# Performance work log

Hardware: AMD Instinct MI355X
Metric: run time of the kernel (lower is better)

The kernel has to match this reference:

```python
import jax, jax.numpy as jnp
import numpy as np

EPS = 1e-5
NEG_SLOPE = 0.01


def _bn(h, gamma, beta):
    # Training-mode batch norm over axis 0 (biased variance, like torch)
    m = h.mean(axis=0)
    v = h.var(axis=0)
    return (h - m) * jax.lax.rsqrt(v + EPS) * gamma + beta


def setup_inputs() -> dict:
    N, F, H, C = 2048, 64, 128, 2
    key = jax.random.key(0)
    ks = jax.random.split(key, 12)
    g = lambda k, shp: jax.random.normal(k, shp, dtype=jnp.float32) * 0.05
    return {
        "x": jax.random.normal(ks[0], (N, F), dtype=jnp.float32),
        "node_features": jax.random.uniform(ks[1], (N, F), dtype=jnp.float32),
        "W1": g(ks[2], (F, H)), "b1": jnp.zeros((H,), jnp.float32),
        "g1": jnp.ones((H,), jnp.float32), "be1": jnp.zeros((H,), jnp.float32),
        "W2": g(ks[3], (H, H)), "b2": jnp.zeros((H,), jnp.float32),
        "g2": jnp.ones((H,), jnp.float32), "be2": jnp.zeros((H,), jnp.float32),
        "W3": g(ks[4], (H, F)), "b3": jnp.zeros((F,), jnp.float32),
        "W5": g(ks[5], (F, H)), "b5": jnp.zeros((H,), jnp.float32),
        "g5": jnp.ones((H,), jnp.float32), "be5": jnp.zeros((H,), jnp.float32),
        "W6": g(ks[6], (H, C)), "b6": jnp.zeros((C,), jnp.float32),
    }


def reference(x, node_features, W1, b1, g1, be1, W2, b2, g2, be2, W3, b3,
              W5, b5, g5, be5, W6, b6):
    N = node_features.shape[0]
    C = W6.shape[1]
    # static upper-triangular edge list == torch.combinations(arange(N), r=2)
    ei, ej = np.triu_indices(N, k=1)

    h = node_features
    xinit = h
    h = _bn(jax.nn.leaky_relu(h @ W1 + b1, NEG_SLOPE), g1, be1)
    h = _bn(jax.nn.leaky_relu(h @ W2 + b2, NEG_SLOPE), g2, be2)
    h = h @ W3 + b3 + xinit  # [N, F]

    # edge prediction: gather pairs, elementwise mult, MLP+BN+softmax
    e = h[ei] * h[ej]  # [E, F]
    e = _bn(jax.nn.leaky_relu(e @ W5 + b5, NEG_SLOPE), g5, be5)
    edge_pred = jax.nn.softmax(e @ W6 + b6, axis=-1)  # [E, C]

    probs = jnp.zeros((N, N, C), dtype=edge_pred.dtype)
    probs = probs.at[ei, ej].set(edge_pred).at[ej, ei].set(edge_pred)
    return probs
```

## Files before the change

### kernel.cpp

```cpp
#include <hip/hip_runtime.h>
#include <hip/hip_bf16.h>


typedef short short8 __attribute__((ext_vector_type(8)));
typedef float floatx4 __attribute__((ext_vector_type(4)));
typedef float float2v __attribute__((ext_vector_type(2)));

#define NN 2048
#define EPSV 1e-5f
#define EDGEF 2096128.f

__device__ __forceinline__ float bf2f(short s) {
    return __uint_as_float(((unsigned)(unsigned short)s) << 16);
}
__device__ __forceinline__ short f2bf(float f) {
    unsigned u = __float_as_uint(f);
    unsigned r = (u + 0x7FFFu + ((u >> 16) & 1u)) >> 16;
    return (short)r;
}
__device__ __forceinline__ float lrelu(float x) { return fmaxf(x, 0.01f * x); }
__device__ __forceinline__ float2v lrelu2(float2v z) {
    float2v r; r.x = fmaxf(z.x, 0.01f * z.x); r.y = fmaxf(z.y, 0.01f * z.y);
    return r;
}
__device__ __forceinline__ float2v fma2(float2v a, float2v b, float2v c) {
    float2v r; r.x = fmaf(a.x, b.x, c.x); r.y = fmaf(a.y, b.y, c.y); return r;
}

__device__ __forceinline__ int physB(int h, int f) {
    return ((((h >> 4) * 2 + (f >> 5)) * 64 + ((f >> 3) & 3) * 16 + (h & 15)) * 8) + (f & 7);
}

__device__ __forceinline__ void decode_tile(int bid, int& i0, int& j0, bool& str) {
    int s = bid >> 3, m = 0;
#pragma unroll 1
    while (s >= 32 - m) { s -= 32 - m; ++m; }
    i0 = ((bid & 7) + (m << 3)) * 8;
    j0 = (m + s) * 64;
    str = (s == 0);
}

__global__ __launch_bounds__(256) void k_l1(const float* __restrict__ nf,
                                            const float* __restrict__ W1,
                                            const float* __restrict__ b1,
                                            const float* __restrict__ W5,
                                            float* __restrict__ act1,
                                            float* __restrict__ stat1,
                                            short* __restrict__ w5bf) {
    __shared__ float xl[8 * 64];
    __shared__ float sS[128], sQ[128];
    int t = threadIdx.x, n0 = blockIdx.x * 8;
    if (blockIdx.x < 32) {
        int idx = blockIdx.x * 256 + t;
        w5bf[physB(idx & 127, idx >> 7)] = f2bf(W5[idx]);
    }
    if (t < 128) { sS[t] = 0.f; sQ[t] = 0.f; }
    xl[t] = nf[(size_t)n0 * 64 + t];
    xl[t + 256] = nf[(size_t)n0 * 64 + t + 256];
    __syncthreads();
    int nl = t >> 5, h0 = (t & 31) * 4;
    float acc[4];
    for (int k = 0; k < 4; ++k) acc[k] = b1[h0 + k];
    for (int f = 0; f < 64; ++f) {
        float r = xl[nl * 64 + f];
        const float* wr = W1 + f * 128 + h0;
        for (int k = 0; k < 4; ++k) acc[k] = fmaf(r, wr[k], acc[k]);
    }
    for (int k = 0; k < 4; ++k) {
        float a = lrelu(acc[k]);
        act1[(size_t)(n0 + nl) * 128 + h0 + k] = a;
        atomicAdd(&sS[h0 + k], a);
        atomicAdd(&sQ[h0 + k], a * a);
    }
    __syncthreads();
    if (t < 128) atomicAdd(&stat1[t], sS[t]);
    else atomicAdd(&stat1[t], sQ[t - 128]);
}

__global__ __launch_bounds__(256) void k_l2(const float* __restrict__ act1,
                                            const float* __restrict__ stat1,
                                            const float* __restrict__ g1,
                                            const float* __restrict__ be1,
                                            const float* __restrict__ W2,
                                            const float* __restrict__ b2,
                                            float* __restrict__ act2,
                                            float* __restrict__ stat2) {
    __shared__ float a1n[8 * 128];
    __shared__ float sS[128], sQ[128];
    int t = threadIdx.x, n0 = blockIdx.x * 8;
    if (t < 128) { sS[t] = 0.f; sQ[t] = 0.f; }
    for (int k = 0; k < 4; ++k) {
        int e = t + 256 * k;
        int nl = e >> 7, h = e & 127;
        float m = stat1[h] * (1.f / 2048.f);
        float v = stat1[128 + h] * (1.f / 2048.f) - m * m;
        float sc = rsqrtf(v + EPSV);
        a1n[e] = (act1[(size_t)(n0 + nl) * 128 + h] - m) * sc * g1[h] + be1[h];
    }
    __syncthreads();
    int nl = t >> 5, h0 = (t & 31) * 4;
    float acc[4];
    for (int k = 0; k < 4; ++k) acc[k] = b2[h0 + k];
    for (int hi = 0; hi < 128; ++hi) {
        float r = a1n[nl * 128 + hi];
        const float* wr = W2 + hi * 128 + h0;
        for (int k = 0; k < 4; ++k) acc[k] = fmaf(r, wr[k], acc[k]);
    }
    for (int k = 0; k < 4; ++k) {
        float a = lrelu(acc[k]);
        act2[(size_t)(n0 + nl) * 128 + h0 + k] = a;
        atomicAdd(&sS[h0 + k], a);
        atomicAdd(&sQ[h0 + k], a * a);
    }
    __syncthreads();
    if (t < 128) atomicAdd(&stat2[t], sS[t]);
    else atomicAdd(&stat2[t], sQ[t - 128]);
}

__global__ __launch_bounds__(256) void k_l3(const float* __restrict__ act2,
                                            const float* __restrict__ stat2,
                                            const float* __restrict__ g2,
                                            const float* __restrict__ be2,
                                            const float* __restrict__ W3,
                                            const float* __restrict__ b3,
                                            const float* __restrict__ nf,
                                            short* __restrict__ hb) {
    __shared__ float a2n[8 * 128];
    int t = threadIdx.x, n0 = blockIdx.x * 8;
    for (int k = 0; k < 4; ++k) {
        int e = t + 256 * k;
        int nl = e >> 7, h = e & 127;
        float m = stat2[h] * (1.f / 2048.f);
        float v = stat2[128 + h] * (1.f / 2048.f) - m * m;
        float sc = rsqrtf(v + EPSV);
        a2n[e] = (act2[(size_t)(n0 + nl) * 128 + h] - m) * sc * g2[h] + be2[h];
    }
    __syncthreads();
    int nl = t >> 5, f0 = (t & 31) * 2;
    float acc[2] = {0.f, 0.f};
    for (int hi = 0; hi < 128; ++hi) {
        float r = a2n[nl * 128 + hi];
        const float* wr = W3 + hi * 64 + f0;
        acc[0] = fmaf(r, wr[0], acc[0]);
        acc[1] = fmaf(r, wr[1], acc[1]);
    }
    float v0 = acc[0] + b3[f0] + nf[(size_t)(n0 + nl) * 64 + f0];
    float v1 = acc[1] + b3[f0 + 1] + nf[(size_t)(n0 + nl) * 64 + f0 + 1];
    unsigned p = (unsigned)(unsigned short)f2bf(v0) |
                 ((unsigned)(unsigned short)f2bf(v1) << 16);
    ((unsigned*)hb)[(size_t)(n0 + nl) * 32 + (f0 >> 1)] = p;
}

__global__ __launch_bounds__(256) void k_bi(const short* __restrict__ w5bf,
                                            const short* __restrict__ hb,
                                            short* __restrict__ T) {
    int b = blockIdx.x, t = threadIdx.x;
    __shared__ short sHi[8 * 64];
    if (t < 64) ((short8*)sHi)[t] = ((const short8*)(hb + (size_t)b * 512))[t];
    __syncthreads();
    for (int i = 0; i < 8; ++i) {
        short8* dst = (short8*)(T + (size_t)(b * 8 + i) * 8192);
#pragma unroll
        for (int k = 0; k < 4; ++k) {
            int c = t + 256 * k;
            int ks = (c >> 6) & 1, quad = (c & 63) >> 4;
            int fb = ks * 32 + quad * 8;
            short8 wv = ((const short8*)w5bf)[c];
            short8 hv = *(const short8*)(sHi + i * 64 + fb);
            short8 ov;
#pragma unroll
            for (int e = 0; e < 8; ++e) ov[e] = f2bf(bf2f(wv[e]) * bf2f(hv[e]));
            dst[c] = ov;
        }
    }
}

__global__ void k_mid(const float* __restrict__ SQe8, const float* __restrict__ W6,
                      const float* __restrict__ b6, const float* __restrict__ g5,
                      const float* __restrict__ be5, float* __restrict__ w6d,
                      float* __restrict__ b6d) {
    __shared__ float part[128];
    int h = threadIdx.x;
    float s = 0.f, q = 0.f;
    for (int x = 0; x < 8; ++x) {
        s += SQe8[x * 256 + h];
        q += SQe8[x * 256 + 128 + h];
    }
    float m = s / EDGEF;
    float v = q / EDGEF - m * m;
    float sc = rsqrtf(v + EPSV);
    float dW = W6[h * 2] - W6[h * 2 + 1];
    float sg = sc * g5[h];
    w6d[h] = sg * dW;
    part[h] = (be5[h] - m * sg) * dW;
    __syncthreads();
    if (h == 0) {
        float acc = b6[0] - b6[1];
        for (int k = 0; k < 128; ++k) acc += part[k];
        b6d[0] = acc;
    }
}

__global__ __launch_bounds__(256, 4) void edge_p1(
    const short* __restrict__ hb, const short* __restrict__ T,
    const float* __restrict__ b5, float* __restrict__ SQe8)
{
    int i0, j0; bool str;
    decode_tile(blockIdx.x, i0, j0, str);

    int t = threadIdx.x, lane = t & 63, w = t >> 6;
    int quad = lane >> 4, col = lane & 15;

    short8 hfr[4][2];
#pragma unroll
    for (int mt = 0; mt < 4; ++mt)
#pragma unroll
        for (int ks = 0; ks < 2; ++ks)
            hfr[mt][ks] = *(const short8*)(hb + (size_t)(j0 + mt * 16 + col) * 64 + ks * 32 + quad * 8);

    const short* Tb = T + (size_t)i0 * 8192;
    int toff[2][2];
#pragma unroll
    for (int n = 0; n < 2; ++n)
#pragma unroll
        for (int ks = 0; ks < 2; ++ks)
            toff[n][ks] = ((((w * 2 + n) * 2 + ks) * 64) + lane) * 8;

    float b5c[2] = { b5[w * 32 + col], b5[w * 32 + 16 + col] };
    float2v S2[2], Q2[2];
#pragma unroll
    for (int n = 0; n < 2; ++n) { S2[n] = 0.f; Q2[n] = 0.f; }

    short8 ta[2][2], tb[2][2];

    auto prefetch = [&](short8 (&dst)[2][2], int i) {
        const short* Tn = Tb + (size_t)i * 8192;
#pragma unroll
        for (int n = 0; n < 2; ++n)
#pragma unroll
            for (int ks = 0; ks < 2; ++ks)
                dst[n][ks] = *(const short8*)(Tn + toff[n][ks]);
    };

    auto bodyC = [&](short8 (&tc)[2][2]) {
#pragma unroll
        for (int n = 0; n < 2; ++n) {
#pragma unroll
            for (int mt = 0; mt < 4; ++mt) {
                floatx4 c = {b5c[n], b5c[n], b5c[n], b5c[n]};
                c = __builtin_amdgcn_mfma_f32_16x16x32_bf16(hfr[mt][0], tc[n][0], c, 0, 0, 0);
                c = __builtin_amdgcn_mfma_f32_16x16x32_bf16(hfr[mt][1], tc[n][1], c, 0, 0, 0);
                float2v z01, z23;
                z01.x = c[0]; z01.y = c[1];
                z23.x = c[2]; z23.y = c[3];
                float2v a01 = lrelu2(z01), a23 = lrelu2(z23);
                S2[n] += a01 + a23;
                Q2[n] = fma2(a01, a01, Q2[n]);
                Q2[n] = fma2(a23, a23, Q2[n]);
            }
        }
    };

    auto bodyM = [&](int i, short8 (&tc)[2][2]) {
        int igi = i0 + i;
#pragma unroll
        for (int n = 0; n < 2; ++n) {
#pragma unroll
            for (int mt = 0; mt < 4; ++mt) {
                floatx4 c = {b5c[n], b5c[n], b5c[n], b5c[n]};
                c = __builtin_amdgcn_mfma_f32_16x16x32_bf16(hfr[mt][0], tc[n][0], c, 0, 0, 0);
                c = __builtin_amdgcn_mfma_f32_16x16x32_bf16(hfr[mt][1], tc[n][1], c, 0, 0, 0);
                int jb = j0 + mt * 16 + quad * 4;
                float2v z01, z23;
                z01.x = (jb + 0 > igi) ? c[0] : 0.f;
                z01.y = (jb + 1 > igi) ? c[1] : 0.f;
                z23.x = (jb + 2 > igi) ? c[2] : 0.f;
                z23.y = (jb + 3 > igi) ? c[3] : 0.f;
                float2v a01 = lrelu2(z01), a23 = lrelu2(z23);
                S2[n] += a01 + a23;
                Q2[n] = fma2(a01, a01, Q2[n]);
                Q2[n] = fma2(a23, a23, Q2[n]);
            }
        }
    };

    prefetch(ta, 0);
    if (!str) {
        for (int ii = 0; ii < 8; ii += 2) {
            prefetch(tb, ii + 1);
            bodyC(ta);
            if (ii + 2 < 8) prefetch(ta, ii + 2);
            bodyC(tb);
        }
    } else {
        for (int ii = 0; ii < 8; ii += 2) {
            prefetch(tb, ii + 1);
            bodyM(ii, ta);
            if (ii + 2 < 8) prefetch(ta, ii + 2);
            bodyM(ii + 1, tb);
        }
    }

    float* dst = SQe8 + (blockIdx.x & 7) * 256;
#pragma unroll
    for (int n = 0; n < 2; ++n) {
        float Sa = S2[n].x + S2[n].y;
        float Qa = Q2[n].x + Q2[n].y;
        Sa += __shfl_xor(Sa, 16); Sa += __shfl_xor(Sa, 32);
        Qa += __shfl_xor(Qa, 16); Qa += __shfl_xor(Qa, 32);
        if (quad == 0) {
            atomicAdd(&dst[w * 32 + n * 16 + col], Sa);
            atomicAdd(&dst[128 + w * 32 + n * 16 + col], Qa);
        }
    }
}

__global__ __launch_bounds__(256, 4) void edge_p2(
    const short* __restrict__ hb, const short* __restrict__ T,
    const float* __restrict__ b5, const float* __restrict__ w6d,
    const float* __restrict__ b6dp, float* __restrict__ out)
{
    int i0, j0; bool str;
    decode_tile(blockIdx.x, i0, j0, str);
    __shared__ float sV[4][8][64];
    __shared__ float sP[8][65];

    int t = threadIdx.x, lane = t & 63, w = t >> 6;
    int quad = lane >> 4, col = lane & 15;

    float bb = b6dp[0];
    float b5q[2][4];
    float2v wq[2][2];
#pragma unroll
    for (int m = 0; m < 2; ++m)
#pragma unroll
        for (int r = 0; r < 4; ++r) {
            int h = w * 32 + m * 16 + quad * 4 + r;
            b5q[m][r] = b5[h];
            ((float*)&wq[m][r >> 1])[r & 1] = w6d[h];
        }

    short8 hfr[4][2];
#pragma unroll
    for (int mt = 0; mt < 4; ++mt)
#pragma unroll
        for (int ks = 0; ks < 2; ++ks)
            hfr[mt][ks] = *(const short8*)(hb + (size_t)(j0 + mt * 16 + col) * 64 + ks * 32 + quad * 8);

    const short* Tb = T + (size_t)i0 * 8192;
    int toff[2][2];
#pragma unroll
    for (int m = 0; m < 2; ++m)
#pragma unroll
        for (int ks = 0; ks < 2; ++ks)
            toff[m][ks] = ((((w * 2 + m) * 2 + ks) * 64) + lane) * 8;

    short8 ta[2][2], tb[2][2];

    auto prefetch = [&](short8 (&dst)[2][2], int i) {
        const short* Tn = Tb + (size_t)i * 8192;
#pragma unroll
        for (int m = 0; m < 2; ++m)
#pragma unroll
            for (int ks = 0; ks < 2; ++ks)
                dst[m][ks] = *(const short8*)(Tn + toff[m][ks]);
    };

    auto body2 = [&](int i, short8 (&tc)[2][2]) {
        float2v acc[4];
#pragma unroll
        for (int k = 0; k < 4; ++k) acc[k] = 0.f;
#pragma unroll
        for (int m = 0; m < 2; ++m) {
#pragma unroll
            for (int nj = 0; nj < 4; ++nj) {
                floatx4 c = {b5q[m][0], b5q[m][1], b5q[m][2], b5q[m][3]};
                c = __builtin_amdgcn_mfma_f32_16x16x32_bf16(tc[m][0], hfr[nj][0], c, 0, 0, 0);
                c = __builtin_amdgcn_mfma_f32_16x16x32_bf16(tc[m][1], hfr[nj][1], c, 0, 0, 0);
                float2v z01, z23;
                z01.x = c[0]; z01.y = c[1];
                z23.x = c[2]; z23.y = c[3];
                acc[nj] = fma2(lrelu2(z01), wq[m][0], acc[nj]);
                acc[nj] = fma2(lrelu2(z23), wq[m][1], acc[nj]);
            }
        }
#pragma unroll
        for (int nj = 0; nj < 4; ++nj) {
            float v = acc[nj].x + acc[nj].y;
            v += __shfl_xor(v, 16);
            v += __shfl_xor(v, 32);
            if (quad == 0) sV[w][i][nj * 16 + col] = v;
        }
    };

    prefetch(ta, 0);
    for (int ii = 0; ii < 8; ii += 2) {
        prefetch(tb, ii + 1);
        body2(ii, ta);
        if (ii + 2 < 8) prefetch(ta, ii + 2);
        body2(ii + 1, tb);
    }
    __syncthreads();

#pragma unroll
    for (int k = 0; k < 2; ++k) {
        int e = t + 256 * k;
        int il = e >> 6, jl = e & 63;
        float v = bb + sV[0][il][jl] + sV[1][il][jl] + sV[2][il][jl] + sV[3][il][jl];
        float p = 1.f / (1.f + __expf(-v));
        sP[il][jl] = p;
        int ig = i0 + il, jg = j0 + jl;
        float2v pr;
        if (!str || jg > ig) {
            pr.x = p; pr.y = 1.f - p;
            *(float2v*)(out + ((size_t)ig * NN + jg) * 2) = pr;
        } else if (jg == ig) {
            pr.x = 0.f; pr.y = 0.f;
            *(float2v*)(out + ((size_t)ig * NN + jg) * 2) = pr;
        }
    }
    __syncthreads();

    if (!str) {
        int jr = t >> 2, f1 = (t & 3) * 4;
        float4 u;
#pragma unroll
        for (int e = 0; e < 4; ++e) {
            int ff = f1 + e;
            float p = sP[ff >> 1][jr];
            ((float*)&u)[e] = (ff & 1) ? 1.f - p : p;
        }
        *(float4*)(out + ((size_t)(j0 + jr) * NN + i0) * 2 + f1) = u;
    } else {
#pragma unroll
        for (int e = 0; e < 4; ++e) {
            int f = t * 4 + e;
            int jr = f >> 4, ff = f & 15;
            int il = ff >> 1, c2 = ff & 1;
            int jg = j0 + jr, ig = i0 + il;
            if (jg > ig) {
                float p = sP[il][jr];
                out[((size_t)jg * NN + ig) * 2 + c2] = c2 ? 1.f - p : p;
            }
        }
    }
}

extern "C" void kernel_launch(void* const* d_in, const int* in_sizes, int n_in,
                              void* d_out, int out_size, void* d_ws, size_t ws_size,
                              hipStream_t stream) {
    const float* nf  = (const float*)d_in[1];
    const float* W1  = (const float*)d_in[2];
    const float* b1  = (const float*)d_in[3];
    const float* g1  = (const float*)d_in[4];
    const float* be1 = (const float*)d_in[5];
    const float* W2  = (const float*)d_in[6];
    const float* b2  = (const float*)d_in[7];
    const float* g2  = (const float*)d_in[8];
    const float* be2 = (const float*)d_in[9];
    const float* W3  = (const float*)d_in[10];
    const float* b3  = (const float*)d_in[11];
    const float* W5  = (const float*)d_in[12];
    const float* b5  = (const float*)d_in[13];
    const float* g5  = (const float*)d_in[14];
    const float* be5 = (const float*)d_in[15];
    const float* W6  = (const float*)d_in[16];
    const float* b6  = (const float*)d_in[17];
    float* out = (float*)d_out;

    float* wsf   = (float*)d_ws;
    float* stat1 = wsf;
    float* stat2 = wsf + 256;
    float* SQe8  = wsf + 512;
    float* w6d   = wsf + 2560;
    float* b6dp  = wsf + 2688;
    float* act1  = wsf + 4096;
    float* act2  = act1 + 262144;
    short* hb    = (short*)(act2 + 262144);
    short* w5bf  = hb + 131072;
    short* Tbuf  = w5bf + 8192;

    hipMemsetAsync(d_ws, 0, 4096 * sizeof(float), stream);

    k_l1<<<256, 256, 0, stream>>>(nf, W1, b1, W5, act1, stat1, w5bf);
    k_l2<<<256, 256, 0, stream>>>(act1, stat1, g1, be1, W2, b2, act2, stat2);
    k_l3<<<256, 256, 0, stream>>>(act2, stat2, g2, be2, W3, b3, nf, hb);
    k_bi<<<256, 256, 0, stream>>>(w5bf, hb, Tbuf);

    edge_p1<<<4224, 256, 0, stream>>>(hb, Tbuf, b5, SQe8);
    k_mid<<<1, 128, 0, stream>>>(SQe8, W6, b6, g5, be5, w6d, b6dp);
    edge_p2<<<4224, 256, 0, stream>>>(hb, Tbuf, b5, w6d, b6dp, out);
}
```

Baseline: 255.9 us.

## Fuse node MLP layers into one cooperative kernel with grid syncs

Merges the three node-MLP kernels and the bilinear T-building kernel into a single cooperative-launch kernel. Per-node activations stay in shared memory across layers, and grid.sync is used for the batch-norm statistics. This removes three launches and the global round-trips for act1, act2 and w5bf. Separately, the launch_bounds occupancy hints on edge_p1 and edge_p2 are raised, which may force register spills in exchange for more resident waves.

```diff
diff --git a/kernel.cpp b/kernel.cpp
--- a/kernel.cpp
+++ b/kernel.cpp
@@ -1,5 +1,8 @@
 #include <hip/hip_runtime.h>
 #include <hip/hip_bf16.h>
+#include <hip/hip_cooperative_groups.h>
+
+namespace cg = cooperative_groups;
 
 
 typedef short short8 __attribute__((ext_vector_type(8)));
@@ -25,6 +28,9 @@
 }
 __device__ __forceinline__ float2v fma2(float2v a, float2v b, float2v c) {
     float2v r; r.x = fmaf(a.x, b.x, c.x); r.y = fmaf(a.y, b.y, c.y); return r;
+}
+__device__ __forceinline__ float aload(const float* p) {
+    return __hip_atomic_load(p, __ATOMIC_RELAXED, __HIP_MEMORY_SCOPE_AGENT);
 }
 
 __device__ __forceinline__ int physB(int h, int f) {
@@ -40,133 +46,143 @@
     str = (s == 0);
 }
 
-__global__ __launch_bounds__(256) void k_l1(const float* __restrict__ nf,
-                                            const float* __restrict__ W1,
-                                            const float* __restrict__ b1,
-                                            const float* __restrict__ W5,
-                                            float* __restrict__ act1,
-                                            float* __restrict__ stat1,
-                                            short* __restrict__ w5bf) {
+__global__ __launch_bounds__(256) void k_node(
+    const float* __restrict__ nf,
+    const float* __restrict__ W1, const float* __restrict__ b1,
+    const float* __restrict__ g1, const float* __restrict__ be1,
+    const float* __restrict__ W2, const float* __restrict__ b2,
+    const float* __restrict__ g2, const float* __restrict__ be2,
+    const float* __restrict__ W3, const float* __restrict__ b3,
+    const float* __restrict__ W5,
+    float* __restrict__ stat1, float* __restrict__ stat2,
+    short* __restrict__ hb, short* __restrict__ T)
+{
+    cg::grid_group grid = cg::this_grid();
+
     __shared__ float xl[8 * 64];
+    __shared__ float sA1[8 * 128];
+    __shared__ float sA2[8 * 128];
+    __shared__ short sW5[8192];
+    __shared__ short sH[8 * 64];
     __shared__ float sS[128], sQ[128];
+    __shared__ float nA[128], nB[128];
+
     int t = threadIdx.x, n0 = blockIdx.x * 8;
-    if (blockIdx.x < 32) {
-        int idx = blockIdx.x * 256 + t;
-        w5bf[physB(idx & 127, idx >> 7)] = f2bf(W5[idx]);
-    }
-    if (t < 128) { sS[t] = 0.f; sQ[t] = 0.f; }
+
+    for (int k = 0; k < 32; ++k) {
+        int idx = t + 256 * k;
+        sW5[physB(idx & 127, idx >> 7)] = f2bf(W5[idx]);
+    }
     xl[t] = nf[(size_t)n0 * 64 + t];
     xl[t + 256] = nf[(size_t)n0 * 64 + t + 256];
-    __syncthreads();
+    if (t < 128) { sS[t] = 0.f; sQ[t] = 0.f; }
+    __syncthreads();
+
     int nl = t >> 5, h0 = (t & 31) * 4;
-    float acc[4];
-    for (int k = 0; k < 4; ++k) acc[k] = b1[h0 + k];
-    for (int f = 0; f < 64; ++f) {
-        float r = xl[nl * 64 + f];
-        const float* wr = W1 + f * 128 + h0;
-        for (int k = 0; k < 4; ++k) acc[k] = fmaf(r, wr[k], acc[k]);
-    }
-    for (int k = 0; k < 4; ++k) {
-        float a = lrelu(acc[k]);
-        act1[(size_t)(n0 + nl) * 128 + h0 + k] = a;
-        atomicAdd(&sS[h0 + k], a);
-        atomicAdd(&sQ[h0 + k], a * a);
+
+    {
+        float acc[4];
+        for (int k = 0; k < 4; ++k) acc[k] = b1[h0 + k];
+        for (int f = 0; f < 64; ++f) {
+            float r = xl[nl * 64 + f];
+            const float* wr = W1 + f * 128 + h0;
+            for (int k = 0; k < 4; ++k) acc[k] = fmaf(r, wr[k], acc[k]);
+        }
+        for (int k = 0; k < 4; ++k) {
+            float a = lrelu(acc[k]);
+            sA1[nl * 128 + h0 + k] = a;
+            atomicAdd(&sS[h0 + k], a);
+            atomicAdd(&sQ[h0 + k], a * a);
+        }
     }
     __syncthreads();
     if (t < 128) atomicAdd(&stat1[t], sS[t]);
-    else atomicAdd(&stat1[t], sQ[t - 128]);
-}
-
-__global__ __launch_bounds__(256) void k_l2(const float* __restrict__ act1,
-                                            const float* __restrict__ stat1,
-                                            const float* __restrict__ g1,
-                                            const float* __restrict__ be1,
-                                            const float* __restrict__ W2,
-                                            const float* __restrict__ b2,
-                                            float* __restrict__ act2,
-                                            float* __restrict__ stat2) {
-    __shared__ float a1n[8 * 128];
-    __shared__ float sS[128], sQ[128];
-    int t = threadIdx.x, n0 = blockIdx.x * 8;
-    if (t < 128) { sS[t] = 0.f; sQ[t] = 0.f; }
+    else atomicAdd(&stat1[128 + (t - 128)], sQ[t - 128]);
+    grid.sync();
+
+    if (t < 128) {
+        float s = aload(stat1 + t);
+        float q = aload(stat1 + 128 + t);
+        float m = s * (1.f / 2048.f);
+        float v = q * (1.f / 2048.f) - m * m;
+        float sc = rsqrtf(v + EPSV) * g1[t];
+        nA[t] = sc;
+        nB[t] = be1[t] - m * sc;
+        sS[t] = 0.f; sQ[t] = 0.f;
+    }
+    __syncthreads();
     for (int k = 0; k < 4; ++k) {
         int e = t + 256 * k;
-        int nl = e >> 7, h = e & 127;
-        float m = stat1[h] * (1.f / 2048.f);
-        float v = stat1[128 + h] * (1.f / 2048.f) - m * m;
-        float sc = rsqrtf(v + EPSV);
-        a1n[e] = (act1[(size_t)(n0 + nl) * 128 + h] - m) * sc * g1[h] + be1[h];
-    }
-    __syncthreads();
-    int nl = t >> 5, h0 = (t & 31) * 4;
-    float acc[4];
-    for (int k = 0; k < 4; ++k) acc[k] = b2[h0 + k];
-    for (int hi = 0; hi < 128; ++hi) {
-        float r = a1n[nl * 128 + hi];
-        const float* wr = W2 + hi * 128 + h0;
-        for (int k = 0; k < 4; ++k) acc[k] = fmaf(r, wr[k], acc[k]);
-    }
-    for (int k = 0; k < 4; ++k) {
-        float a = lrelu(acc[k]);
-        act2[(size_t)(n0 + nl) * 128 + h0 + k] = a;
-        atomicAdd(&sS[h0 + k], a);
-        atomicAdd(&sQ[h0 + k], a * a);
+        int h = e & 127;
+        sA1[e] = sA1[e] * nA[h] + nB[h];
+    }
+    __syncthreads();
+
+    {
+        float acc[4];
+        for (int k = 0; k < 4; ++k) acc[k] = b2[h0 + k];
+        for (int hi = 0; hi < 128; ++hi) {
+            float r = sA1[nl * 128 + hi];
+            const float* wr = W2 + hi * 128 + h0;
+            for (int k = 0; k < 4; ++k) acc[k] = fmaf(r, wr[k], acc[k]);
+        }
+        for (int k = 0; k < 4; ++k) {
+            float a = lrelu(acc[k]);
+            sA2[nl * 128 + h0 + k] = a;
+            atomicAdd(&sS[h0 + k], a);
+            atomicAdd(&sQ[h0 + k], a * a);
+        }
     }
     __syncthreads();
     if (t < 128) atomicAdd(&stat2[t], sS[t]);
-    else atomicAdd(&stat2[t], sQ[t - 128]);
-}
-
-__global__ __launch_bounds__(256) void k_l3(const float* __restrict__ act2,
-                                            const float* __restrict__ stat2,
-                                            const float* __restrict__ g2,
-                                            const float* __restrict__ be2,
-                                            const float* __restrict__ W3,
-                                            const float* __restrict__ b3,
-                                            const float* __restrict__ nf,
-                                            short* __restrict__ hb) {
-    __shared__ float a2n[8 * 128];
-    int t = threadIdx.x, n0 = blockIdx.x * 8;
+    else atomicAdd(&stat2[128 + (t - 128)], sQ[t - 128]);
+    grid.sync();
+
+    if (t < 128) {
+        float s = aload(stat2 + t);
+        float q = aload(stat2 + 128 + t);
+        float m = s * (1.f / 2048.f);
+        float v = q * (1.f / 2048.f) - m * m;
+        float sc = rsqrtf(v + EPSV) * g2[t];
+        nA[t] = sc;
+        nB[t] = be2[t] - m * sc;
+    }
+    __syncthreads();
     for (int k = 0; k < 4; ++k) {
         int e = t + 256 * k;
-        int nl = e >> 7, h = e & 127;
-        float m = stat2[h] * (1.f / 2048.f);
-        float v = stat2[128 + h] * (1.f / 2048.f) - m * m;
-        float sc = rsqrtf(v + EPSV);
-        a2n[e] = (act2[(size_t)(n0 + nl) * 128 + h] - m) * sc * g2[h] + be2[h];
-    }
-    __syncthreads();
-    int nl = t >> 5, f0 = (t & 31) * 2;
-    float acc[2] = {0.f, 0.f};
-    for (int hi = 0; hi < 128; ++hi) {
-        float r = a2n[nl * 128 + hi];
-        const float* wr = W3 + hi * 64 + f0;
-        acc[0] = fmaf(r, wr[0], acc[0]);
-        acc[1] = fmaf(r, wr[1], acc[1]);
-    }
-    float v0 = acc[0] + b3[f0] + nf[(size_t)(n0 + nl) * 64 + f0];
-    float v1 = acc[1] + b3[f0 + 1] + nf[(size_t)(n0 + nl) * 64 + f0 + 1];
-    unsigned p = (unsigned)(unsigned short)f2bf(v0) |
-                 ((unsigned)(unsigned short)f2bf(v1) << 16);
-    ((unsigned*)hb)[(size_t)(n0 + nl) * 32 + (f0 >> 1)] = p;
-}
-
-__global__ __launch_bounds__(256) void k_bi(const short* __restrict__ w5bf,
-                                            const short* __restrict__ hb,
-                                            short* __restrict__ T) {
-    int b = blockIdx.x, t = threadIdx.x;
-    __shared__ short sHi[8 * 64];
-    if (t < 64) ((short8*)sHi)[t] = ((const short8*)(hb + (size_t)b * 512))[t];
-    __syncthreads();
+        int h = e & 127;
+        sA2[e] = sA2[e] * nA[h] + nB[h];
+    }
+    __syncthreads();
+
+    {
+        int f0 = (t & 31) * 2;
+        float acc0 = 0.f, acc1 = 0.f;
+        for (int hi = 0; hi < 128; ++hi) {
+            float r = sA2[nl * 128 + hi];
+            const float* wr = W3 + hi * 64 + f0;
+            acc0 = fmaf(r, wr[0], acc0);
+            acc1 = fmaf(r, wr[1], acc1);
+        }
+        float v0 = acc0 + b3[f0] + xl[nl * 64 + f0];
+        float v1 = acc1 + b3[f0 + 1] + xl[nl * 64 + f0 + 1];
+        short s0 = f2bf(v0), s1 = f2bf(v1);
+        sH[nl * 64 + f0] = s0;
+        sH[nl * 64 + f0 + 1] = s1;
+        unsigned p = (unsigned)(unsigned short)s0 | ((unsigned)(unsigned short)s1 << 16);
+        ((unsigned*)hb)[(size_t)(n0 + nl) * 32 + (f0 >> 1)] = p;
+    }
+    __syncthreads();
+
     for (int i = 0; i < 8; ++i) {
-        short8* dst = (short8*)(T + (size_t)(b * 8 + i) * 8192);
+        short8* dst = (short8*)(T + (size_t)(n0 + i) * 8192);
 #pragma unroll
         for (int k = 0; k < 4; ++k) {
             int c = t + 256 * k;
             int ks = (c >> 6) & 1, quad = (c & 63) >> 4;
             int fb = ks * 32 + quad * 8;
-            short8 wv = ((const short8*)w5bf)[c];
-            short8 hv = *(const short8*)(sHi + i * 64 + fb);
+            short8 wv = ((const short8*)sW5)[c];
+            short8 hv = *(const short8*)(sH + i * 64 + fb);
             short8 ov;
 #pragma unroll
             for (int e = 0; e < 8; ++e) ov[e] = f2bf(bf2f(wv[e]) * bf2f(hv[e]));
@@ -201,7 +217,7 @@
     }
 }
 
-__global__ __launch_bounds__(256, 4) void edge_p1(
+__global__ __launch_bounds__(256, 8) void edge_p1(
     const short* __restrict__ hb, const short* __restrict__ T,
     const float* __restrict__ b5, float* __restrict__ SQe8)
 {
@@ -315,7 +331,7 @@
     }
 }
 
-__global__ __launch_bounds__(256, 4) void edge_p2(
+__global__ __launch_bounds__(256, 6) void edge_p2(
     const short* __restrict__ hb, const short* __restrict__ T,
     const float* __restrict__ b5, const float* __restrict__ w6d,
     const float* __restrict__ b6dp, float* __restrict__ out)
@@ -474,18 +490,21 @@
     float* SQe8  = wsf + 512;
     float* w6d   = wsf + 2560;
     float* b6dp  = wsf + 2688;
-    float* act1  = wsf + 4096;
-    float* act2  = act1 + 262144;
-    short* hb    = (short*)(act2 + 262144);
-    short* w5bf  = hb + 131072;
-    short* Tbuf  = w5bf + 8192;
+    short* hb    = (short*)(wsf + 4096);
+    short* Tbuf  = hb + 131072;
 
     hipMemsetAsync(d_ws, 0, 4096 * sizeof(float), stream);
 
-    k_l1<<<256, 256, 0, stream>>>(nf, W1, b1, W5, act1, stat1, w5bf);
-    k_l2<<<256, 256, 0, stream>>>(act1, stat1, g1, be1, W2, b2, act2, stat2);
-    k_l3<<<256, 256, 0, stream>>>(act2, stat2, g2, be2, W3, b3, nf, hb);
-    k_bi<<<256, 256, 0, stream>>>(w5bf, hb, Tbuf);
+    {
+        void* args[] = {
+            (void*)&nf, (void*)&W1, (void*)&b1, (void*)&g1, (void*)&be1,
+            (void*)&W2, (void*)&b2, (void*)&g2, (void*)&be2,
+            (void*)&W3, (void*)&b3, (void*)&W5,
+            (void*)&stat1, (void*)&stat2, (void*)&hb, (void*)&Tbuf
+        };
+        hipLaunchCooperativeKernel((void*)k_node, dim3(256), dim3(256),
+                                   args, 0, stream);
+    }
 
     edge_p1<<<4224, 256, 0, stream>>>(hb, Tbuf, b5, SQe8);
     k_mid<<<1, 128, 0, stream>>>(SQe8, W6, b6, g5, be5, w6d, b6dp);
```

After: 973.7 us. 281% more time.
